# Optimization experiments

Measured on AMD Instinct MI355X. Metric: run time of the kernel, lower is better.

## Reference

```python
import jax, jax.numpy as jnp
import numpy as np

LN_EPS = 1e-12


def setup_inputs() -> dict:
    key = jax.random.key(0)
    ks = jax.random.split(key, 5)
    B, N, D_IN, D_OUT, E = 32, 2048, 128, 128, 64
    return {
        "x": jax.random.normal(ks[0], (B, N, D_IN), dtype=jnp.float32),
        "node_embeddings": jax.random.normal(ks[1], (N, E), dtype=jnp.float32),
        "time_embeddings": jax.random.normal(ks[2], (E,), dtype=jnp.float32),
        "weights_pool": jax.random.normal(ks[3], (E, 2, D_IN, D_OUT), dtype=jnp.float32) * 0.02,
        "bias_pool": jax.random.normal(ks[4], (E, D_OUT), dtype=jnp.float32) * 0.02,
        "ln_weight": jnp.ones((E,), dtype=jnp.float32),
        "ln_bias": jnp.zeros((E,), dtype=jnp.float32),
    }


def reference(x, node_embeddings, time_embeddings, weights_pool, bias_pool, ln_weight, ln_bias):
    # e: [N, E] = LayerNorm(node_emb + time_emb)  (dropout in eval mode = identity)
    e = node_embeddings + time_embeddings[None, :]
    mu = jnp.mean(e, axis=-1, keepdims=True)
    var = jnp.mean(jnp.square(e - mu), axis=-1, keepdims=True)
    e = (e - mu) * jax.lax.rsqrt(var + LN_EPS) * ln_weight + ln_bias

    # adaptive adjacency: softmax over rows of e @ e.T  -> [N, N]
    adj = jax.nn.softmax(jnp.einsum('nd,md->nm', e, e), axis=1)

    # per-node weights [N, 2, I, O] and bias [N, O]
    weights = jnp.einsum('nd,dkio->nkio', e, weights_pool)
    bias = e @ bias_pool  # [N, O]

    # supports: k=0 identity (x itself), k=1 adjacency aggregation
    x_agg = jnp.einsum('nm,bmc->bnc', adj, x)        # [B, N, I]
    x_g = jnp.stack([x, x_agg], axis=2)              # [B, N, 2, I]

    # per-node batched GEMM + bias
    out = jnp.einsum('bnki,nkio->bno', x_g, weights) + bias
    return out
```

## Files before the change

### kernel.cpp

```cpp
#include <hip/hip_runtime.h>


typedef unsigned short u16;
typedef unsigned int u32;
typedef __attribute__((ext_vector_type(8))) short bf16x8;
typedef __attribute__((ext_vector_type(4))) float f32x4;
typedef const __attribute__((address_space(1))) u16* gas1;
typedef __attribute__((address_space(3))) u16* las3;

#define NN 2048
#define EE 64
#define CC 128
#define BB 32

__device__ __forceinline__ u16 f2bf(float f) {
  u32 u = __builtin_bit_cast(u32, f);
  u += 0x7fffu + ((u >> 16) & 1u);
  return (u16)(u >> 16);
}

__device__ __forceinline__ f32x4 mfma16(bf16x8 a, bf16x8 b, f32x4 c) {
  return __builtin_amdgcn_mfma_f32_16x16x32_bf16(a, b, c, 0, 0, 0);
}

__global__ __launch_bounds__(256) void k_mega0(
    const float* __restrict__ x, const float* __restrict__ ne,
    const float* __restrict__ te, const float* __restrict__ pool,
    const float* __restrict__ bias_pool, const float* __restrict__ lnw,
    const float* __restrict__ lnb,
    float* __restrict__ e, u16* __restrict__ e_bf, float* __restrict__ bias_out,
    u16* __restrict__ pool_r, u16* __restrict__ x_t, u16* __restrict__ xg_t) {
  __shared__ __align__(16) char smem[33280];
  int bid = blockIdx.x;
  int tid = threadIdx.x;
  if (bid < 512) {
    float* sh = (float*)smem;
    int nw = tid >> 6, d = tid & 63;
    int n = bid * 4 + nw;
    float v = ne[n * EE + d] + te[d];
    float s = v;
#pragma unroll
    for (int off = 32; off > 0; off >>= 1) s += __shfl_xor(s, off);
    float mean = s * (1.0f / 64.0f);
    float c = v - mean;
    float q = c * c;
#pragma unroll
    for (int off = 32; off > 0; off >>= 1) q += __shfl_xor(q, off);
    float inv = rsqrtf(q * (1.0f / 64.0f) + 1e-12f);
    float ev = c * inv * lnw[d] + lnb[d];
    e[n * EE + d] = ev;
    e_bf[n * EE + d] = f2bf(ev);
    sh[nw * 64 + d] = ev;
    __syncthreads();
#pragma unroll
    for (int oo = 0; oo < 2; ++oo) {
      int o = oo * 64 + d;
      float acc = 0.f;
#pragma unroll 8
      for (int dd = 0; dd < 64; ++dd) acc += sh[nw * 64 + dd] * bias_pool[dd * CC + o];
      bias_out[n * CC + o] = acc;
    }
  } else if (bid < 768) {
    float* t = (float*)smem;
    int ki = bid - 512;
    for (int it = 0; it < 32; ++it) {
      int idx = it * 256 + tid;
      int d = idx >> 7, o = idx & 127;
      t[o * 65 + d] = pool[d * 32768 + ki * 128 + o];
    }
    __syncthreads();
    for (int it = 0; it < 32; ++it) {
      int idx = it * 256 + tid;
      int o = idx >> 6, d = idx & 63;
      pool_r[((size_t)o * 256 + ki) * 64 + d] = f2bf(t[o * 65 + d]);
    }
  } else {
    u16* t = (u16*)smem;
    int bx = bid - 768;
    int b = bx >> 5;
    int m0 = (bx & 31) * 64;
    for (int it = 0; it < 32; ++it) {
      int idx = it * 256 + tid;
      int m = idx >> 7, c = idx & 127;
      float v = x[((size_t)b * NN + m0 + m) * CC + c];
      t[c * 68 + m] = f2bf(v);
    }
    __syncthreads();
    for (int it = 0; it < 32; ++it) {
      int idx = it * 256 + tid;
      int c = idx >> 6, m = idx & 63;
      x_t[((size_t)b * CC + c) * NN + m0 + m] = t[c * 68 + m];
    }
    for (int it = 0; it < 16; ++it) {
      int idx = it * 256 + tid;
      int m = idx >> 6, c2 = idx & 63;
      float2 v = *(const float2*)&x[((size_t)b * NN + m0 + m) * CC + c2 * 2];
      u32 pk = (u32)f2bf(v.x) | ((u32)f2bf(v.y) << 16);
      *(u32*)&xg_t[(((size_t)(m0 + m)) * 32 + b) * 256 + c2 * 2] = pk;
    }
  }
}

__global__ __launch_bounds__(256) void k_Sexp(const float* __restrict__ e,
                                              u16* __restrict__ P,
                                              float* __restrict__ rs) {
  __shared__ float er[64 * 68];
  __shared__ float ec[64 * 68];
  int n0 = (blockIdx.x >> 5) * 64, m0 = (blockIdx.x & 31) * 64;
  int tid = threadIdx.x;
  for (int it = 0; it < 16; ++it) {
    int idx = it * 256 + tid;
    int r = idx >> 6, d = idx & 63;
    er[r * 68 + d] = e[(n0 + r) * EE + d];
    ec[r * 68 + d] = e[(m0 + r) * EE + d];
  }
  __syncthreads();
  int tx = tid & 15, ty = tid >> 4;
  float acc[4][4] = {};
  for (int d4 = 0; d4 < 64; d4 += 4) {
    f32x4 av[4], bv[4];
#pragma unroll
    for (int i = 0; i < 4; ++i) av[i] = *(const f32x4*)&er[(ty + 16 * i) * 68 + d4];
#pragma unroll
    for (int j = 0; j < 4; ++j) bv[j] = *(const f32x4*)&ec[(tx + 16 * j) * 68 + d4];
#pragma unroll
    for (int i = 0; i < 4; ++i)
#pragma unroll
      for (int j = 0; j < 4; ++j) {
        acc[i][j] += av[i][0] * bv[j][0];
        acc[i][j] += av[i][1] * bv[j][1];
        acc[i][j] += av[i][2] * bv[j][2];
        acc[i][j] += av[i][3] * bv[j][3];
      }
  }
#pragma unroll
  for (int i = 0; i < 4; ++i) {
    float s = 0.f;
#pragma unroll
    for (int j = 0; j < 4; ++j) {
      float pv = __expf(acc[i][j]);
      P[(size_t)(n0 + ty + 16 * i) * NN + m0 + tx + 16 * j] = f2bf(pv);
      s += pv;
    }
#pragma unroll
    for (int off = 8; off > 0; off >>= 1) s += __shfl_xor(s, off);
    if (tx == 0) atomicAdd(&rs[n0 + ty + 16 * i], s);
  }
}

__global__ __launch_bounds__(256, 4) void k_mega2(
    const u16* __restrict__ P, const u16* __restrict__ x_t,
    const float* __restrict__ rs, u16* __restrict__ xg_t,
    const u16* __restrict__ e_bf, const u16* __restrict__ pool_r,
    u16* __restrict__ W_t) {
  __shared__ __align__(16) char smem[33792];
  int tid = threadIdx.x;
  int lane = tid & 63, w = tid >> 6;
  int lm = lane & 15, lq = lane >> 4;
  if (blockIdx.x < 512) {
    u16* As = (u16*)smem;
    u16* Bs = (u16*)(smem + 16384);
    int mb = blockIdx.x & 15, b = blockIdx.x >> 4;
    int n0 = mb * 128;
    int wm = w >> 1, wn = w & 1;
    f32x4 acc[4][4] = {};
    const u16* a_src = P + (size_t)n0 * NN;
    const u16* b_src = x_t + (size_t)b * CC * NN;
    for (int kc = 0; kc < NN; kc += 64) {
      __syncthreads();
#pragma unroll
      for (int ii = 0; ii < 4; ++ii) {
        int idx = ii * 256 + tid;
        int row = idx >> 3, ch = idx & 7;
        __builtin_amdgcn_global_load_lds((gas1)(a_src + (size_t)row * NN + kc + ch * 8),
                                         (las3)(As + (size_t)(ii * 256 + w * 64) * 8), 16, 0, 0);
        __builtin_amdgcn_global_load_lds((gas1)(b_src + (size_t)row * NN + kc + ch * 8),
                                         (las3)(Bs + (size_t)(ii * 256 + w * 64) * 8), 16, 0, 0);
      }
      __syncthreads();
#pragma unroll
      for (int kk = 0; kk < 64; kk += 32) {
        bf16x8 af[4], bq[4];
#pragma unroll
        for (int i = 0; i < 4; ++i)
          af[i] = *(const bf16x8*)&As[(wm * 64 + i * 16 + lm) * 64 + kk + lq * 8];
#pragma unroll
        for (int j = 0; j < 4; ++j)
          bq[j] = *(const bf16x8*)&Bs[(wn * 64 + j * 16 + lm) * 64 + kk + lq * 8];
#pragma unroll
        for (int i = 0; i < 4; ++i)
#pragma unroll
          for (int j = 0; j < 4; ++j)
            acc[i][j] = mfma16(af[i], bq[j], acc[i][j]);
      }
    }
#pragma unroll
    for (int i = 0; i < 4; ++i) {
      int nr = n0 + wm * 64 + i * 16 + lq * 4;
#pragma unroll
      for (int r = 0; r < 4; ++r) {
        float sc = 1.0f / rs[nr + r];
#pragma unroll
        for (int j = 0; j < 4; ++j) {
          int c = wn * 64 + j * 16 + lm;
          xg_t[((size_t)(nr + r) * 32 + b) * 256 + 128 + c] = f2bf(acc[i][j][r] * sc);
        }
      }
    }
  } else {
    u16* Tl = (u16*)smem;
    int bid = blockIdx.x - 512;
    int cb = bid & 127, nb = bid >> 7;
    int c0 = cb * 256, n0 = nb * 64;
    bf16x8 eB[4][2];
#pragma unroll
    for (int nt = 0; nt < 4; ++nt)
#pragma unroll
      for (int ks = 0; ks < 2; ++ks)
        eB[nt][ks] = *(const bf16x8*)&e_bf[(n0 + nt * 16 + lm) * EE + ks * 32 + lq * 8];
#pragma unroll
    for (int ct = 0; ct < 4; ++ct) {
      int ctile = w * 4 + ct;
      const u16* ap = pool_r + ((size_t)c0 + ctile * 16 + lm) * 64 + lq * 8;
      bf16x8 pA0 = *(const bf16x8*)ap;
      bf16x8 pA1 = *(const bf16x8*)(ap + 32);
#pragma unroll
      for (int nt = 0; nt < 4; ++nt) {
        f32x4 g = {0.f, 0.f, 0.f, 0.f};
        g = mfma16(pA0, eB[nt][0], g);
        g = mfma16(pA1, eB[nt][1], g);
        ushort4 h;
        h.x = f2bf(g[0]); h.y = f2bf(g[1]); h.z = f2bf(g[2]); h.w = f2bf(g[3]);
        *(ushort4*)&Tl[(nt * 16 + lm) * 264 + ctile * 16 + lq * 4] = h;
      }
    }
    __syncthreads();
#pragma unroll
    for (int it = 0; it < 8; ++it) {
      int idx = it * 256 + tid;
      int node = idx >> 5, seg = idx & 31;
      uint4 v = *(const uint4*)&Tl[node * 264 + seg * 8];
      *(uint4*)&W_t[(size_t)(n0 + node) * 32768 + c0 + seg * 8] = v;
    }
  }
}

__global__ __launch_bounds__(256, 3) void k_apply(const u16* __restrict__ xg_t,
                                                  const u16* __restrict__ W_t,
                                                  const float* __restrict__ bias,
                                                  float* __restrict__ out) {
  int n0 = blockIdx.x * 2;
  int tid = threadIdx.x;
  int lane = tid & 63, w = tid >> 6;
  int lm = lane & 15, lq = lane >> 4;
  int n = n0 + (w & 1), oh = w >> 1;
  const u16* xb = xg_t + (size_t)n * 32 * 256;
  const u16* wb = W_t + (size_t)n * 32768 + (size_t)oh * 64 * 256;
  f32x4 acc[2][4] = {};
#pragma unroll
  for (int ks = 0; ks < 8; ++ks) {
    int ko = ks * 32 + lq * 8;
    bf16x8 a0 = *(const bf16x8*)&xb[lm * 256 + ko];
    bf16x8 a1 = *(const bf16x8*)&xb[(16 + lm) * 256 + ko];
#pragma unroll
    for (int ot = 0; ot < 4; ++ot) {
      bf16x8 bv = *(const bf16x8*)&wb[(ot * 16 + lm) * 256 + ko];
      acc[0][ot] = mfma16(a0, bv, acc[0][ot]);
      acc[1][ot] = mfma16(a1, bv, acc[1][ot]);
    }
  }
#pragma unroll
  for (int ot = 0; ot < 4; ++ot) {
    int oc = oh * 64 + ot * 16 + lm;
    float bv = bias[n * CC + oc];
#pragma unroll
    for (int mt = 0; mt < 2; ++mt)
#pragma unroll
      for (int r = 0; r < 4; ++r) {
        int b = mt * 16 + lq * 4 + r;
        out[((size_t)b * NN + n) * CC + oc] = acc[mt][ot][r] + bv;
      }
  }
}

extern "C" void kernel_launch(void* const* d_in, const int* in_sizes, int n_in,
                              void* d_out, int out_size, void* d_ws, size_t ws_size,
                              hipStream_t stream) {
  const float* x        = (const float*)d_in[0];
  const float* node_emb = (const float*)d_in[1];
  const float* time_emb = (const float*)d_in[2];
  const float* pool     = (const float*)d_in[3];
  const float* bias_pl  = (const float*)d_in[4];
  const float* ln_w     = (const float*)d_in[5];
  const float* ln_b     = (const float*)d_in[6];
  float* out = (float*)d_out;

  char* p = (char*)d_ws;
  auto alloc = [&](size_t bytes) {
    char* r = p;
    p += (bytes + 255) & ~(size_t)255;
    return r;
  };
  float* e      = (float*)alloc((size_t)NN * EE * 4);
  u16*   e_bf   = (u16*)  alloc((size_t)NN * EE * 2);
  float* biasb  = (float*)alloc((size_t)NN * CC * 4);
  u16*   Pm     = (u16*)  alloc((size_t)NN * NN * 2);
  float* rs     = (float*)alloc((size_t)NN * 4);
  u16*   x_t    = (u16*)  alloc((size_t)BB * CC * NN * 2);
  u16*   xg_t   = (u16*)  alloc((size_t)NN * BB * 256 * 2);
  u16*   pool_r = (u16*)  alloc((size_t)128 * 256 * 64 * 2);
  u16*   W_t    = (u16*)  alloc((size_t)NN * 32768 * 2);

  if (ws_size < (size_t)(p - (char*)d_ws)) return;

  (void)hipMemsetAsync(rs, 0, (size_t)NN * 4, stream);

  k_mega0<<<1792, 256, 0, stream>>>(x, node_emb, time_emb, pool, bias_pl, ln_w, ln_b,
                                    e, e_bf, biasb, pool_r, x_t, xg_t);
  k_Sexp<<<1024, 256, 0, stream>>>(e, Pm, rs);
  k_mega2<<<4608, 256, 0, stream>>>(Pm, x_t, rs, xg_t, e_bf, pool_r, W_t);
  k_apply<<<NN / 2, 256, 0, stream>>>(xg_t, W_t, biasb, out);
}
```

Measured before the change: 238.4 us.

## Fuse per-node weight generation into apply kernel, dropping W_t global buffer

```diff
diff --git a/kernel.cpp b/kernel.cpp
--- a/kernel.cpp
+++ b/kernel.cpp
@@ -148,138 +148,134 @@
   }
 }
 
-__global__ __launch_bounds__(256, 4) void k_mega2(
+__global__ __launch_bounds__(256, 4) void k_aggr(
     const u16* __restrict__ P, const u16* __restrict__ x_t,
-    const float* __restrict__ rs, u16* __restrict__ xg_t,
-    const u16* __restrict__ e_bf, const u16* __restrict__ pool_r,
-    u16* __restrict__ W_t) {
-  __shared__ __align__(16) char smem[33792];
+    const float* __restrict__ rs, u16* __restrict__ xg_t) {
+  __shared__ __align__(16) char smem[32768];
   int tid = threadIdx.x;
   int lane = tid & 63, w = tid >> 6;
   int lm = lane & 15, lq = lane >> 4;
-  if (blockIdx.x < 512) {
-    u16* As = (u16*)smem;
-    u16* Bs = (u16*)(smem + 16384);
-    int mb = blockIdx.x & 15, b = blockIdx.x >> 4;
-    int n0 = mb * 128;
-    int wm = w >> 1, wn = w & 1;
-    f32x4 acc[4][4] = {};
-    const u16* a_src = P + (size_t)n0 * NN;
-    const u16* b_src = x_t + (size_t)b * CC * NN;
-    for (int kc = 0; kc < NN; kc += 64) {
-      __syncthreads();
-#pragma unroll
-      for (int ii = 0; ii < 4; ++ii) {
-        int idx = ii * 256 + tid;
-        int row = idx >> 3, ch = idx & 7;
-        __builtin_amdgcn_global_load_lds((gas1)(a_src + (size_t)row * NN + kc + ch * 8),
-                                         (las3)(As + (size_t)(ii * 256 + w * 64) * 8), 16, 0, 0);
-        __builtin_amdgcn_global_load_lds((gas1)(b_src + (size_t)row * NN + kc + ch * 8),
-                                         (las3)(Bs + (size_t)(ii * 256 + w * 64) * 8), 16, 0, 0);
+  u16* As = (u16*)smem;
+  u16* Bs = (u16*)(smem + 16384);
+  int mb = blockIdx.x & 15, b = blockIdx.x >> 4;
+  int n0 = mb * 128;
+  int wm = w >> 1, wn = w & 1;
+  f32x4 acc[4][4] = {};
+  const u16* a_src = P + (size_t)n0 * NN;
+  const u16* b_src = x_t + (size_t)b * CC * NN;
+  for (int kc = 0; kc < NN; kc += 64) {
+    __syncthreads();
+#pragma unroll
+    for (int ii = 0; ii < 4; ++ii) {
+      int idx = ii * 256 + tid;
+      int row = idx >> 3, ch = idx & 7;
+      __builtin_amdgcn_global_load_lds((gas1)(a_src + (size_t)row * NN + kc + ch * 8),
+                                       (las3)(As + (size_t)(ii * 256 + w * 64) * 8), 16, 0, 0);
+      __builtin_amdgcn_global_load_lds((gas1)(b_src + (size_t)row * NN + kc + ch * 8),
+                                       (las3)(Bs + (size_t)(ii * 256 + w * 64) * 8), 16, 0, 0);
+    }
+    __syncthreads();
+#pragma unroll
+    for (int kk = 0; kk < 64; kk += 32) {
+      bf16x8 af[4], bq[4];
+#pragma unroll
+      for (int i = 0; i < 4; ++i)
+        af[i] = *(const bf16x8*)&As[(wm * 64 + i * 16 + lm) * 64 + kk + lq * 8];
+#pragma unroll
+      for (int j = 0; j < 4; ++j)
+        bq[j] = *(const bf16x8*)&Bs[(wn * 64 + j * 16 + lm) * 64 + kk + lq * 8];
+#pragma unroll
+      for (int i = 0; i < 4; ++i)
+#pragma unroll
+        for (int j = 0; j < 4; ++j)
+          acc[i][j] = mfma16(af[i], bq[j], acc[i][j]);
+    }
+  }
+#pragma unroll
+  for (int i = 0; i < 4; ++i) {
+    int nr = n0 + wm * 64 + i * 16 + lq * 4;
+#pragma unroll
+    for (int r = 0; r < 4; ++r) {
+      float sc = 1.0f / rs[nr + r];
+#pragma unroll
+      for (int j = 0; j < 4; ++j) {
+        int c = wn * 64 + j * 16 + lm;
+        xg_t[((size_t)(nr + r) * 32 + b) * 256 + 128 + c] = f2bf(acc[i][j][r] * sc);
       }
-      __syncthreads();
-#pragma unroll
-      for (int kk = 0; kk < 64; kk += 32) {
-        bf16x8 af[4], bq[4];
-#pragma unroll
-        for (int i = 0; i < 4; ++i)
-          af[i] = *(const bf16x8*)&As[(wm * 64 + i * 16 + lm) * 64 + kk + lq * 8];
-#pragma unroll
-        for (int j = 0; j < 4; ++j)
-          bq[j] = *(const bf16x8*)&Bs[(wn * 64 + j * 16 + lm) * 64 + kk + lq * 8];
-#pragma unroll
-        for (int i = 0; i < 4; ++i)
-#pragma unroll
-          for (int j = 0; j < 4; ++j)
-            acc[i][j] = mfma16(af[i], bq[j], acc[i][j]);
-      }
-    }
-#pragma unroll
-    for (int i = 0; i < 4; ++i) {
-      int nr = n0 + wm * 64 + i * 16 + lq * 4;
-#pragma unroll
-      for (int r = 0; r < 4; ++r) {
-        float sc = 1.0f / rs[nr + r];
-#pragma unroll
-        for (int j = 0; j < 4; ++j) {
-          int c = wn * 64 + j * 16 + lm;
-          xg_t[((size_t)(nr + r) * 32 + b) * 256 + 128 + c] = f2bf(acc[i][j][r] * sc);
-        }
-      }
-    }
-  } else {
-    u16* Tl = (u16*)smem;
-    int bid = blockIdx.x - 512;
-    int cb = bid & 127, nb = bid >> 7;
-    int c0 = cb * 256, n0 = nb * 64;
-    bf16x8 eB[4][2];
-#pragma unroll
-    for (int nt = 0; nt < 4; ++nt)
-#pragma unroll
-      for (int ks = 0; ks < 2; ++ks)
-        eB[nt][ks] = *(const bf16x8*)&e_bf[(n0 + nt * 16 + lm) * EE + ks * 32 + lq * 8];
-#pragma unroll
-    for (int ct = 0; ct < 4; ++ct) {
-      int ctile = w * 4 + ct;
-      const u16* ap = pool_r + ((size_t)c0 + ctile * 16 + lm) * 64 + lq * 8;
-      bf16x8 pA0 = *(const bf16x8*)ap;
-      bf16x8 pA1 = *(const bf16x8*)(ap + 32);
-#pragma unroll
-      for (int nt = 0; nt < 4; ++nt) {
-        f32x4 g = {0.f, 0.f, 0.f, 0.f};
-        g = mfma16(pA0, eB[nt][0], g);
-        g = mfma16(pA1, eB[nt][1], g);
-        ushort4 h;
-        h.x = f2bf(g[0]); h.y = f2bf(g[1]); h.z = f2bf(g[2]); h.w = f2bf(g[3]);
-        *(ushort4*)&Tl[(nt * 16 + lm) * 264 + ctile * 16 + lq * 4] = h;
-      }
-    }
-    __syncthreads();
-#pragma unroll
-    for (int it = 0; it < 8; ++it) {
-      int idx = it * 256 + tid;
-      int node = idx >> 5, seg = idx & 31;
-      uint4 v = *(const uint4*)&Tl[node * 264 + seg * 8];
-      *(uint4*)&W_t[(size_t)(n0 + node) * 32768 + c0 + seg * 8] = v;
-    }
-  }
-}
-
-__global__ __launch_bounds__(256, 3) void k_apply(const u16* __restrict__ xg_t,
-                                                  const u16* __restrict__ W_t,
-                                                  const float* __restrict__ bias,
-                                                  float* __restrict__ out) {
-  int n0 = blockIdx.x * 2;
+    }
+  }
+}
+
+#define GA_OS 40
+#define GA_NS 648
+__global__ __launch_bounds__(256) void k_genapply(
+    const u16* __restrict__ e_bf, const u16* __restrict__ pool_r,
+    const u16* __restrict__ xg_t, const float* __restrict__ biasb,
+    float* __restrict__ out) {
+  __shared__ u16 W[32 * GA_NS];
   int tid = threadIdx.x;
   int lane = tid & 63, w = tid >> 6;
   int lm = lane & 15, lq = lane >> 4;
-  int n = n0 + (w & 1), oh = w >> 1;
-  const u16* xb = xg_t + (size_t)n * 32 * 256;
-  const u16* wb = W_t + (size_t)n * 32768 + (size_t)oh * 64 * 256;
-  f32x4 acc[2][4] = {};
-#pragma unroll
-  for (int ks = 0; ks < 8; ++ks) {
-    int ko = ks * 32 + lq * 8;
-    bf16x8 a0 = *(const bf16x8*)&xb[lm * 256 + ko];
-    bf16x8 a1 = *(const bf16x8*)&xb[(16 + lm) * 256 + ko];
+  int ng = blockIdx.x & 63, og = blockIdx.x >> 6;
+  int n0 = ng * 32, o0 = og * 16;
+
+  bf16x8 eB[2][2];
+#pragma unroll
+  for (int nc = 0; nc < 2; ++nc)
+#pragma unroll
+    for (int ks = 0; ks < 2; ++ks)
+      eB[nc][ks] = *(const bf16x8*)&e_bf[(n0 + nc * 16 + lm) * EE + ks * 32 + lq * 8];
+
+  f32x4 acc[8][2] = {};
+  for (int kt = 0; kt < 8; ++kt) {
+    int ki0 = kt * 32;
+    if (kt) __syncthreads();
 #pragma unroll
     for (int ot = 0; ot < 4; ++ot) {
-      bf16x8 bv = *(const bf16x8*)&wb[(ot * 16 + lm) * 256 + ko];
-      acc[0][ot] = mfma16(a0, bv, acc[0][ot]);
-      acc[1][ot] = mfma16(a1, bv, acc[1][ot]);
-    }
-  }
-#pragma unroll
-  for (int ot = 0; ot < 4; ++ot) {
-    int oc = oh * 64 + ot * 16 + lm;
-    float bv = bias[n * CC + oc];
-#pragma unroll
-    for (int mt = 0; mt < 2; ++mt)
-#pragma unroll
-      for (int r = 0; r < 4; ++r) {
-        int b = mt * 16 + lq * 4 + r;
-        out[((size_t)b * NN + n) * CC + oc] = acc[mt][ot][r] + bv;
+      int o_l = w * 4 + ot;
+      const u16* pb = pool_r + ((size_t)(o0 + o_l) * 256 + ki0 + lm) * 64 + lq * 8;
+#pragma unroll
+      for (int kc = 0; kc < 2; ++kc) {
+        const u16* ap = pb + kc * 16 * 64;
+        bf16x8 a0 = *(const bf16x8*)ap;
+        bf16x8 a1 = *(const bf16x8*)(ap + 32);
+#pragma unroll
+        for (int nc = 0; nc < 2; ++nc) {
+          f32x4 d = {0.f, 0.f, 0.f, 0.f};
+          d = mfma16(a0, eB[nc][0], d);
+          d = mfma16(a1, eB[nc][1], d);
+          ushort4 h;
+          h.x = f2bf(d[0]); h.y = f2bf(d[1]); h.z = f2bf(d[2]); h.w = f2bf(d[3]);
+          *(ushort4*)&W[(nc * 16 + lm) * GA_NS + o_l * GA_OS + kc * 16 + lq * 4] = h;
+        }
       }
+    }
+    __syncthreads();
+#pragma unroll
+    for (int i = 0; i < 8; ++i) {
+      int n_l = w * 8 + i;
+      bf16x8 wA = *(const bf16x8*)&W[n_l * GA_NS + lm * GA_OS + lq * 8];
+      const u16* xp = xg_t + ((size_t)(n0 + n_l) * 32) * 256 + ki0 + lq * 8;
+      bf16x8 x0 = *(const bf16x8*)(xp + lm * 256);
+      bf16x8 x1 = *(const bf16x8*)(xp + (16 + lm) * 256);
+      acc[i][0] = mfma16(wA, x0, acc[i][0]);
+      acc[i][1] = mfma16(wA, x1, acc[i][1]);
+    }
+  }
+#pragma unroll
+  for (int i = 0; i < 8; ++i) {
+    int n = n0 + w * 8 + i;
+    float4 bv = *(const float4*)&biasb[n * CC + o0 + lq * 4];
+#pragma unroll
+    for (int bt = 0; bt < 2; ++bt) {
+      int b = bt * 16 + lm;
+      float4 o4;
+      o4.x = acc[i][bt][0] + bv.x;
+      o4.y = acc[i][bt][1] + bv.y;
+      o4.z = acc[i][bt][2] + bv.z;
+      o4.w = acc[i][bt][3] + bv.w;
+      *(float4*)&out[((size_t)b * NN + n) * CC + o0 + lq * 4] = o4;
+    }
   }
 }
 
@@ -309,7 +305,6 @@
   u16*   x_t    = (u16*)  alloc((size_t)BB * CC * NN * 2);
   u16*   xg_t   = (u16*)  alloc((size_t)NN * BB * 256 * 2);
   u16*   pool_r = (u16*)  alloc((size_t)128 * 256 * 64 * 2);
-  u16*   W_t    = (u16*)  alloc((size_t)NN * 32768 * 2);
 
   if (ws_size < (size_t)(p - (char*)d_ws)) return;
 
@@ -318,6 +313,6 @@
   k_mega0<<<1792, 256, 0, stream>>>(x, node_emb, time_emb, pool, bias_pl, ln_w, ln_b,
                                     e, e_bf, biasb, pool_r, x_t, xg_t);
   k_Sexp<<<1024, 256, 0, stream>>>(e, Pm, rs);
-  k_mega2<<<4608, 256, 0, stream>>>(Pm, x_t, rs, xg_t, e_bf, pool_r, W_t);
-  k_apply<<<NN / 2, 256, 0, stream>>>(xg_t, W_t, biasb, out);
-}
+  k_aggr<<<512, 256, 0, stream>>>(Pm, x_t, rs, xg_t);
+  k_genapply<<<512, 256, 0, stream>>>(e_bf, pool_r, xg_t, biasb, out);
+}
```

Measured after the change: 247.2 us. 1.04x slower.

## Swizzle LDS tiles, reorder block mapping, and repack per-node weights for contiguous reads

Applied to the files above, without the earlier changes.

```diff
diff --git a/kernel.cpp b/kernel.cpp
--- a/kernel.cpp
+++ b/kernel.cpp
@@ -152,7 +152,7 @@
     const u16* __restrict__ P, const u16* __restrict__ x_t,
     const float* __restrict__ rs, u16* __restrict__ xg_t,
     const u16* __restrict__ e_bf, const u16* __restrict__ pool_r,
-    u16* __restrict__ W_t) {
+    u16* __restrict__ W_p) {
   __shared__ __align__(16) char smem[33792];
   int tid = threadIdx.x;
   int lane = tid & 63, w = tid >> 6;
@@ -160,7 +160,7 @@
   if (blockIdx.x < 512) {
     u16* As = (u16*)smem;
     u16* Bs = (u16*)(smem + 16384);
-    int mb = blockIdx.x & 15, b = blockIdx.x >> 4;
+    int b = blockIdx.x & 31, mb = blockIdx.x >> 5;
     int n0 = mb * 128;
     int wm = w >> 1, wn = w & 1;
     f32x4 acc[4][4] = {};
@@ -172,21 +172,27 @@
       for (int ii = 0; ii < 4; ++ii) {
         int idx = ii * 256 + tid;
         int row = idx >> 3, ch = idx & 7;
-        __builtin_amdgcn_global_load_lds((gas1)(a_src + (size_t)row * NN + kc + ch * 8),
+        int sc = kc + ((ch ^ (row & 7)) << 3);
+        __builtin_amdgcn_global_load_lds((gas1)(a_src + (size_t)row * NN + sc),
                                          (las3)(As + (size_t)(ii * 256 + w * 64) * 8), 16, 0, 0);
-        __builtin_amdgcn_global_load_lds((gas1)(b_src + (size_t)row * NN + kc + ch * 8),
+        __builtin_amdgcn_global_load_lds((gas1)(b_src + (size_t)row * NN + sc),
                                          (las3)(Bs + (size_t)(ii * 256 + w * 64) * 8), 16, 0, 0);
       }
       __syncthreads();
 #pragma unroll
       for (int kk = 0; kk < 64; kk += 32) {
+        int cb = (kk >> 3) + lq;
         bf16x8 af[4], bq[4];
 #pragma unroll
-        for (int i = 0; i < 4; ++i)
-          af[i] = *(const bf16x8*)&As[(wm * 64 + i * 16 + lm) * 64 + kk + lq * 8];
-#pragma unroll
-        for (int j = 0; j < 4; ++j)
-          bq[j] = *(const bf16x8*)&Bs[(wn * 64 + j * 16 + lm) * 64 + kk + lq * 8];
+        for (int i = 0; i < 4; ++i) {
+          int row = wm * 64 + i * 16 + lm;
+          af[i] = *(const bf16x8*)&As[row * 64 + ((cb ^ (row & 7)) << 3)];
+        }
+#pragma unroll
+        for (int j = 0; j < 4; ++j) {
+          int row = wn * 64 + j * 16 + lm;
+          bq[j] = *(const bf16x8*)&Bs[row * 64 + ((cb ^ (row & 7)) << 3)];
+        }
 #pragma unroll
         for (int i = 0; i < 4; ++i)
 #pragma unroll
@@ -240,13 +246,13 @@
       int idx = it * 256 + tid;
       int node = idx >> 5, seg = idx & 31;
       uint4 v = *(const uint4*)&Tl[node * 264 + seg * 8];
-      *(uint4*)&W_t[(size_t)(n0 + node) * 32768 + c0 + seg * 8] = v;
+      *(uint4*)&W_p[(size_t)(n0 + node) * 32768 + (seg >> 2) * 4096 + cb * 32 + (seg & 3) * 8] = v;
     }
   }
 }
 
 __global__ __launch_bounds__(256, 3) void k_apply(const u16* __restrict__ xg_t,
-                                                  const u16* __restrict__ W_t,
+                                                  const u16* __restrict__ W_p,
                                                   const float* __restrict__ bias,
                                                   float* __restrict__ out) {
   int n0 = blockIdx.x * 2;
@@ -255,7 +261,7 @@
   int lm = lane & 15, lq = lane >> 4;
   int n = n0 + (w & 1), oh = w >> 1;
   const u16* xb = xg_t + (size_t)n * 32 * 256;
-  const u16* wb = W_t + (size_t)n * 32768 + (size_t)oh * 64 * 256;
+  const u16* wb = W_p + (size_t)n * 32768 + (size_t)oh * 64 * 32;
   f32x4 acc[2][4] = {};
 #pragma unroll
   for (int ks = 0; ks < 8; ++ks) {
@@ -264,7 +270,7 @@
     bf16x8 a1 = *(const bf16x8*)&xb[(16 + lm) * 256 + ko];
 #pragma unroll
     for (int ot = 0; ot < 4; ++ot) {
-      bf16x8 bv = *(const bf16x8*)&wb[(ot * 16 + lm) * 256 + ko];
+      bf16x8 bv = *(const bf16x8*)&wb[(size_t)ks * 4096 + (ot * 16 + lm) * 32 + lq * 8];
       acc[0][ot] = mfma16(a0, bv, acc[0][ot]);
       acc[1][ot] = mfma16(a1, bv, acc[1][ot]);
     }
@@ -309,7 +315,7 @@
   u16*   x_t    = (u16*)  alloc((size_t)BB * CC * NN * 2);
   u16*   xg_t   = (u16*)  alloc((size_t)NN * BB * 256 * 2);
   u16*   pool_r = (u16*)  alloc((size_t)128 * 256 * 64 * 2);
-  u16*   W_t    = (u16*)  alloc((size_t)NN * 32768 * 2);
+  u16*   W_p    = (u16*)  alloc((size_t)NN * 32768 * 2);
 
   if (ws_size < (size_t)(p - (char*)d_ws)) return;
 
@@ -318,6 +324,6 @@
   k_mega0<<<1792, 256, 0, stream>>>(x, node_emb, time_emb, pool, bias_pl, ln_w, ln_b,
                                     e, e_bf, biasb, pool_r, x_t, xg_t);
   k_Sexp<<<1024, 256, 0, stream>>>(e, Pm, rs);
-  k_mega2<<<4608, 256, 0, stream>>>(Pm, x_t, rs, xg_t, e_bf, pool_r, W_t);
-  k_apply<<<NN / 2, 256, 0, stream>>>(xg_t, W_t, biasb, out);
-}
+  k_mega2<<<4608, 256, 0, stream>>>(Pm, x_t, rs, xg_t, e_bf, pool_r, W_p);
+  k_apply<<<NN / 2, 256, 0, stream>>>(xg_t, W_p, biasb, out);
+}
```

Result: faster. 230.0 us (-3.5%).
